# Optimization experiments

Measured on AMD Instinct MI355X. Metric: run time of the kernel, lower is better.

Reference implementation:

```python
import jax, jax.numpy as jnp
import numpy as np

B = 128      # graphs
N = 32       # atoms per graph (fixed)
NODES = B * N
E = B * N * N  # fully-connected edges incl. self-loops
H = 256      # hidden_dim
TD = 128     # time_dim
TYPE = 100   # type_dim
NF = 10      # frac_emb_freq
EDGE_DIM = NF * 2 * 3 + 6  # 66
L = 4        # num_layers
EPS = 1e-5


def _edges():
    idx = jnp.arange(NODES).reshape(B, N)
    ei = jnp.broadcast_to(idx[:, :, None], (B, N, N)).reshape(-1)  # row (target)
    ej = jnp.broadcast_to(idx[:, None, :], (B, N, N)).reshape(-1)  # col (source)
    return ei, ej


def _layernorm(x, g, b):
    mu = jnp.mean(x, axis=-1, keepdims=True)
    var = jnp.mean((x - mu) ** 2, axis=-1, keepdims=True)
    return (x - mu) * jax.lax.rsqrt(var + EPS) * g + b


def setup_inputs() -> dict:
    key = jax.random.key(0)
    ks = jax.random.split(key, 32)
    p = lambda k, shp: (jax.random.normal(k, shp, dtype=jnp.float32) * 0.02)
    inp = {
        "t": jax.random.uniform(ks[0], (B,), dtype=jnp.float32),
        "atom_types": jax.random.normal(ks[1], (NODES, TYPE), dtype=jnp.float32),
        "frac_coords": jax.random.uniform(ks[2], (NODES, 3), dtype=jnp.float32),
        "l_polar": jax.random.normal(ks[3], (B, 6), dtype=jnp.float32),
        "node2graph": jnp.repeat(jnp.arange(B, dtype=jnp.int32), N),
        # type_smooth
        "Ws": p(ks[4], (TYPE, H)), "bs": jnp.zeros((H,), jnp.float32),
        # node_embedding
        "Wn": p(ks[5], (H + TD, H)), "bn": jnp.zeros((H,), jnp.float32),
        # per-layer params, stacked over L
        "ln_g": jnp.ones((L, H), jnp.float32), "ln_b": jnp.zeros((L, H), jnp.float32),
        "m1_W": p(ks[6], (L, 2 * H + EDGE_DIM, H)), "m1_b": jnp.zeros((L, H), jnp.float32),
        "m2_W": p(ks[7], (L, H, H)), "m2_b": jnp.zeros((L, H), jnp.float32),
        "a1_W": p(ks[8], (L, 2 * H, H)), "a1_b": jnp.zeros((L, H), jnp.float32),
        "a2_W": p(ks[9], (L, H, H)), "a2_b": jnp.zeros((L, H), jnp.float32),
        # final layer norm + readouts
        "fln_g": jnp.ones((H,), jnp.float32), "fln_b": jnp.zeros((H,), jnp.float32),
        "type_W": p(ks[10], (H, TYPE)), "type_b": jnp.zeros((TYPE,), jnp.float32),
        "polar_W": p(ks[11], (H, 6)),
        "frac_W": p(ks[12], (H, 3)),
    }
    return inp


def reference(t, atom_types, frac_coords, l_polar, node2graph,
              Ws, bs, Wn, bn, ln_g, ln_b, m1_W, m1_b, m2_W, m2_b,
              a1_W, a1_b, a2_W, a2_b, fln_g, fln_b, type_W, type_b,
              polar_W, frac_W):
    ei, ej = _edges()
    edge2graph = node2graph[ei]

    # ---- node features: type_smooth + sinusoidal time embedding ----
    half = TD // 2
    tfreq = jnp.exp(jnp.arange(half, dtype=jnp.float32) * (-np.log(10000.0) / (half - 1)))
    targ = t[:, None] * tfreq[None, :]                       # [B, half]
    time_emb = jnp.concatenate([jnp.sin(targ), jnp.cos(targ)], axis=-1)  # [B, TD]
    time_emb = jnp.repeat(time_emb, N, axis=0)               # [NODES, TD]
    type_emb = atom_types @ Ws + bs                           # [NODES, H]
    nf = jnp.concatenate([type_emb, time_emb], axis=-1) @ Wn + bn  # [NODES, H]

    # ---- edge features: sinusoidal frac-diff embedding + l_polar ----
    d = jnp.mod(frac_coords[ej] - frac_coords[ei], 1.0)       # [E, 3]
    ffreq = 2.0 * np.pi * jnp.arange(NF, dtype=jnp.float32)
    femb = (d[:, :, None] * ffreq[None, None, :]).reshape(E, NF * 3)
    femb = jnp.concatenate([jnp.sin(femb), jnp.cos(femb)], axis=-1)  # [E, 60]
    ef = jnp.concatenate([femb, l_polar[edge2graph]], axis=-1)       # [E, 66]

    # ---- GNN layers ----
    ones = jnp.ones((E,), jnp.float32)
    cnt = jax.ops.segment_sum(ones, ei, num_segments=NODES)          # [NODES]
    cnt = jnp.maximum(cnt, 1.0)[:, None]
    for i in range(L):
        h = _layernorm(nf, ln_g[i], ln_b[i])
        mij = jnp.concatenate([h[ei], h[ej], ef], axis=-1)           # [E, 2H+66]
        mij = jax.nn.silu(mij @ m1_W[i] + m1_b[i])
        mij = jax.nn.silu(mij @ m2_W[i] + m2_b[i])                   # [E, H]
        msg = jax.ops.segment_sum(mij, ei, num_segments=NODES) / cnt  # scatter-mean
        a = jnp.concatenate([nf, msg], axis=-1)
        a = jax.nn.silu(a @ a1_W[i] + a1_b[i])
        a = jax.nn.silu(a @ a2_W[i] + a2_b[i])
        nf = nf + a

    nf = _layernorm(nf, fln_g, fln_b)
    gsum = jax.ops.segment_sum(nf, node2graph, num_segments=B)
    gcnt = jnp.maximum(jax.ops.segment_sum(jnp.ones((NODES,), jnp.float32), node2graph, num_segments=B), 1.0)
    graph_features = gsum / gcnt[:, None]

    type_pred = nf @ type_W + type_b
    l_polar_pred = graph_features @ polar_W
    frac_coords_pred = nf @ frac_W
    return type_pred, l_polar_pred, frac_coords_pred
```

## Files before the change

kernel.cpp:

```cpp
#include <hip/hip_runtime.h>
#include <hip/hip_bf16.h>

typedef __attribute__((ext_vector_type(8))) short short8;
typedef __attribute__((ext_vector_type(4))) short short4v;
typedef __attribute__((ext_vector_type(4))) float float4v;
typedef __bf16 bf16x8 __attribute__((ext_vector_type(8)));

#define MFMA16(A,B,C) __builtin_amdgcn_mfma_f32_16x16x32_bf16( \
    __builtin_bit_cast(bf16x8,(A)), __builtin_bit_cast(bf16x8,(B)), (C), 0, 0, 0)

static __device__ __forceinline__ float bf2f(unsigned short b){
  unsigned u = ((unsigned)b) << 16; float f; __builtin_memcpy(&f,&u,sizeof(f)); return f;
}
static __device__ __forceinline__ unsigned short f2bf(float f){
  unsigned u; __builtin_memcpy(&u,&f,sizeof(u));
  u = (u + 0x7FFFu + ((u>>16)&1u)) >> 16; return (unsigned short)u;
}
static __device__ __forceinline__ float siluf(float x){
  return x * __builtin_amdgcn_rcpf(1.0f + __expf(-x));
}
static __device__ __forceinline__ float ldf(const float* p, size_t i){ return p[i]; }
static __device__ __forceinline__ float ldf(const unsigned short* p, size_t i){ return bf2f(p[i]); }

__global__ __launch_bounds__(256) void k_gemm(
    const unsigned short* __restrict__ A, int lda,
    const unsigned short* __restrict__ Bp, int KT, int NT,
    const float* __restrict__ bias,
    float* __restrict__ outF, int ldoF,
    unsigned short* __restrict__ outH, int ldoH,
    const float* __restrict__ res,
    int Nc, int flags)
{
  const int w = threadIdx.x >> 6, lane = threadIdx.x & 63;
  const int l15 = lane & 15, q = lane >> 4;
  const int rowL = blockIdx.x * 64 + w * 16;
  const int colB = blockIdx.y * 64;
  const short8* pa = (const short8*)(A + (size_t)(rowL + l15) * lda);
  const short8* pb = (const short8*)Bp;
  float4v acc[4] = {};
  int ntc[4];
  #pragma unroll
  for (int i = 0; i < 4; ++i){ int t = (colB >> 4) + i; ntc[i] = t < NT ? t : NT - 1; }
  for (int kt = 0; kt < KT; ++kt){
    short8 a = pa[kt * 4 + q];
    #pragma unroll
    for (int i = 0; i < 4; ++i){
      short8 b = pb[(size_t)(kt * NT + ntc[i]) * 64 + lane];
      acc[i] = MFMA16(a, b, acc[i]);
    }
  }
  const bool doB = flags & 2, doS = flags & 1, doR = flags & 4;
  #pragma unroll
  for (int i = 0; i < 4; ++i){
    int c = colB + i * 16 + l15;
    if (c >= Nc) continue;
    float bv = doB ? bias[c] : 0.0f;
    #pragma unroll
    for (int r = 0; r < 4; ++r){
      int row = rowL + q * 4 + r;
      float v = acc[i][r] + bv;
      if (doS) v = siluf(v);
      if (doR) v += res[(size_t)row * ldoF + c];
      if (outF) outF[(size_t)row * ldoF + c] = v;
      if (outH) outH[(size_t)row * ldoH + c] = f2bf(v);
    }
  }
}

template<typename T>
static __device__ __forceinline__ void pack_tile(
    const T* W, int ldw, int Krows, int Ncols,
    unsigned short* dst, int NTtot, int ntoff, int kt, int nt,
    const float* addrow)
{
  int lane = threadIdx.x;
  int l15 = lane & 15, q = lane >> 4;
  int col = nt * 16 + l15;
  int kr0 = kt * 32 + q * 8;
  short8 v;
  #pragma unroll
  for (int j = 0; j < 8; ++j){
    int r = kr0 + j;
    float x = 0.0f;
    if (r < Krows && col < Ncols){
      x = ldf(W, (size_t)r * ldw + col);
      if (addrow) x += addrow[(r >> 5) * 256 + col];
    }
    v[j] = (short)f2bf(x);
  }
  ((short8*)dst)[(size_t)(kt * NTtot + ntoff + nt) * 64 + lane] = v;
}

__global__ void k_packW(
    const float* Ws, const float* Wn,
    const float* typeW, const float* polarW, const float* fracW,
    const float* m1W, const float* m2W, const float* a1W, const float* a2W,
    unsigned short* Wsp, unsigned short* Wnp, unsigned short* typep,
    unsigned short* polarp, unsigned short* fracp,
    unsigned short* W12p, unsigned short* W1botp, unsigned short* W2Tp,
    unsigned short* a1p, unsigned short* a2p)
{
  int b = blockIdx.x;
  if (b < 64)      { pack_tile(Ws,    256, 100, 256, Wsp,   16, 0, b >> 4, b & 15, nullptr); return; }
  if (b < 256){ int s = b - 64;  pack_tile(Wn,    256, 384, 256, Wnp,   16, 0, s >> 4, s & 15, nullptr); return; }
  if (b < 312){ int s = b - 256; pack_tile(typeW, 100, 256, 100, typep,  7, 0, s / 7,  s % 7,  nullptr); return; }
  if (b < 320){ int s = b - 312; pack_tile(polarW,  6, 256,   6, polarp, 1, 0, s, 0, nullptr); return; }
  if (b < 328){ int s = b - 320; pack_tile(fracW,   3, 256,   3, fracp,  1, 0, s, 0, nullptr); return; }
  int s2 = b - 328;
  int l = s2 / 800, bb = s2 % 800;
  const float* m1Wl = m1W + (size_t)l * 578 * 256;
  const float* m2Wl = m2W + (size_t)l * 65536;
  const float* a1Wl = a1W + (size_t)l * 131072;
  const float* a2Wl = a2W + (size_t)l * 65536;
  unsigned short* W12pl   = W12p   + (size_t)l * 131072;
  unsigned short* W1botpl = W1botp + (size_t)l * 16384;
  unsigned short* W2Tpl   = W2Tp   + (size_t)l * 65536;
  unsigned short* a1pl    = a1p    + (size_t)l * 131072;
  unsigned short* a2pl    = a2p    + (size_t)l * 65536;
  if (bb < 128)       pack_tile(m1Wl,           256, 256, 256, W12pl,  32,  0, bb >> 4, bb & 15, nullptr);
  else if (bb < 256){ int s = bb - 128; pack_tile(m1Wl + 256*256, 256, 256, 256, W12pl,  32, 16, s >> 4, s & 15, nullptr); }
  else if (bb < 288){ int s = bb - 256; pack_tile(m1Wl + 512*256, 256,  64, 256, W1botpl,16,  0, s >> 4, s & 15, nullptr); }
  else if (bb < 416){ int s = bb - 288; pack_tile(m2Wl,           256, 256, 256, W2Tpl,  16,  0, s >> 4, s & 15, nullptr); }
  else if (bb < 672){ int s = bb - 416; pack_tile(a1Wl,           256, 512, 256, a1pl,   16,  0, s >> 4, s & 15, nullptr); }
  else              { int s = bb - 672; pack_tile(a2Wl,           256, 256, 256, a2pl,   16,  0, s >> 4, s & 15, nullptr); }
}

__global__ void k_prep2(const float* at, const float* t, const float* fc,
                        const float* lpol, const float* m1W, const float* m1b,
                        unsigned short* atp, unsigned short* cat1,
                        unsigned short* femb, float* lpw)
{
  int b = blockIdx.x;
  if (b < 2048){
    int id = b * 256 + threadIdx.x;
    int r = id >> 7, c = id & 127;
    atp[id] = (c < 100) ? f2bf(at[r * 100 + c]) : (unsigned short)0;
  } else if (b < 2176){
    int g = b - 2048, i = threadIdx.x;
    if (i < 128){
      float tg = t[g];
      int f = i & 63;
      float fr = __expf((-9.210340371976184f / 63.0f) * (float)f);
      float arg = tg * fr;
      float v = (i < 64) ? __sinf(arg) : __cosf(arg);
      unsigned short hv = f2bf(v);
      for (int n = 0; n < 32; ++n)
        cat1[(size_t)(g * 32 + n) * 384 + 256 + i] = hv;
    }
  } else if (b < 2688){
    int e = (b - 2176) * 256 + threadIdx.x;
    int g = e >> 10, i = (e >> 5) & 31, j = e & 31;
    int nt = g * 32 + i, ns = g * 32 + j;
    unsigned short o[64];
    #pragma unroll
    for (int k = 0; k < 3; ++k){
      float d = fc[ns * 3 + k] - fc[nt * 3 + k];
      d -= floorf(d);
      #pragma unroll
      for (int f = 0; f < 10; ++f){
        float ang = d * (6.283185307179586f * (float)f);
        o[k * 10 + f]      = f2bf(__sinf(ang));
        o[30 + k * 10 + f] = f2bf(__cosf(ang));
      }
    }
    #pragma unroll
    for (int z = 60; z < 64; ++z) o[z] = 0;
    short8* dst = (short8*)(femb + (size_t)e * 64);
    #pragma unroll
    for (int v = 0; v < 8; ++v){
      short8 s;
      #pragma unroll
      for (int j2 = 0; j2 < 8; ++j2) s[j2] = (short)o[v * 8 + j2];
      dst[v] = s;
    }
  } else {
    int s = b - 2688;
    int l = s >> 7, g = s & 127, c = threadIdx.x;
    const float* W = m1W + (size_t)l * 578 * 256;
    float acc = m1b[l * 256 + c];
    #pragma unroll
    for (int k = 0; k < 6; ++k)
      acc += lpol[g * 6 + k] * W[(572 + k) * 256 + c];
    lpw[((size_t)l * 128 + g) * 256 + c] = acc;
  }
}

#define HLD 264

__global__ __launch_bounds__(256) void k_lnP(
    const float* __restrict__ nf, const float* __restrict__ g_,
    const float* __restrict__ b_,
    const unsigned short* __restrict__ W12p, const float* __restrict__ lpwl,
    unsigned short* __restrict__ P1Tp, unsigned short* __restrict__ P2Tp)
{
  __shared__ unsigned short hld[32 * HLD];
  __shared__ unsigned short PT[256 * 40];
  const int w = threadIdx.x >> 6, lane = threadIdx.x & 63;
  const int l15 = lane & 15, q = lane >> 4;
  const int g = blockIdx.x >> 1, halfT = blockIdx.x & 1;
  #pragma unroll
  for (int rr = 0; rr < 8; ++rr){
    int row = w * 8 + rr;
    float4v x = *(const float4v*)(nf + ((size_t)(g*32+row))*256 + lane*4);
    float s = x[0]+x[1]+x[2]+x[3];
    #pragma unroll
    for (int m=1;m<64;m<<=1) s += __shfl_xor(s,m,64);
    float mu = s * (1.f/256.f);
    float d0=x[0]-mu,d1=x[1]-mu,d2=x[2]-mu,d3=x[3]-mu;
    float vs=d0*d0+d1*d1+d2*d2+d3*d3;
    #pragma unroll
    for (int m=1;m<64;m<<=1) vs += __shfl_xor(vs,m,64);
    float rs = rsqrtf(vs*(1.f/256.f)+1e-5f);
    float4v gg = *(const float4v*)(g_ + lane*4);
    float4v bb = *(const float4v*)(b_ + lane*4);
    short4v o;
    o[0]=(short)f2bf(d0*rs*gg[0]+bb[0]);
    o[1]=(short)f2bf(d1*rs*gg[1]+bb[1]);
    o[2]=(short)f2bf(d2*rs*gg[2]+bb[2]);
    o[3]=(short)f2bf(d3*rs*gg[3]+bb[3]);
    *(short4v*)(&hld[row*HLD + lane*4]) = o;
  }
  __syncthreads();
  float4v acc[2][4] = {};
  const short8* pb = (const short8*)W12p;
  for (int kt = 0; kt < 8; ++kt){
    short8 a0 = *(const short8*)(&hld[(size_t)l15*HLD + kt*32 + q*8]);
    short8 a1 = *(const short8*)(&hld[(size_t)(16+l15)*HLD + kt*32 + q*8]);
    #pragma unroll
    for (int i = 0; i < 4; ++i){
      short8 bfr = pb[(size_t)(kt*32 + halfT*16 + w*4 + i)*64 + lane];
      acc[0][i] = MFMA16(a0, bfr, acc[0][i]);
      acc[1][i] = MFMA16(a1, bfr, acc[1][i]);
    }
  }
  #pragma unroll
  for (int i = 0; i < 4; ++i){
    int Tl = w*4 + i;
    float lv = (halfT == 0) ? lpwl[g*256 + Tl*16 + l15] : 0.0f;
    #pragma unroll
    for (int mt = 0; mt < 2; ++mt){
      short4v o;
      #pragma unroll
      for (int r = 0; r < 4; ++r) o[r] = (short)f2bf(acc[mt][i][r] + lv);
      *(short4v*)(&PT[(size_t)(Tl*16 + l15)*40 + mt*16 + q*4]) = o;
    }
  }
  __syncthreads();
  unsigned short* dstbase = halfT ? P2Tp : P1Tp;
  #pragma unroll
  for (int s = 0; s < 4; ++s){
    int Tl = w + s*4;
    short8 v = *(const short8*)(&PT[(size_t)(Tl*16 + l15)*40 + q*8]);
    *(short8*)(dstbase + ((size_t)(g*16 + Tl)*64 + lane)*8) = v;
  }
}

__global__ __launch_bounds__(256) void k_a12(
    const unsigned short* __restrict__ cat2,
    const unsigned short* __restrict__ a1pl, const float* __restrict__ a1bl,
    const unsigned short* __restrict__ a2pl, const float* __restrict__ a2bl,
    float* __restrict__ nf, unsigned short* __restrict__ cat2w)
{
  __shared__ unsigned short t1[16 * HLD];
  const int w = threadIdx.x >> 6, lane = threadIdx.x & 63;
  const int l15 = lane & 15, q = lane >> 4;
  const int r0 = blockIdx.x * 16;
  const short8* pb1 = (const short8*)a1pl;
  const short8* pb2 = (const short8*)a2pl;
  float4v acc[4] = {};
  for (int kt = 0; kt < 16; ++kt){
    short8 a0 = *(const short8*)(cat2 + (size_t)(r0 + l15)*512 + kt*32 + q*8);
    #pragma unroll
    for (int i = 0; i < 4; ++i){
      short8 bfr = pb1[(size_t)(kt*16 + w*4 + i)*64 + lane];
      acc[i] = MFMA16(a0, bfr, acc[i]);
    }
  }
  #pragma unroll
  for (int i = 0; i < 4; ++i){
    int c = (w*4+i)*16 + l15;
    float bv = a1bl[c];
    #pragma unroll
    for (int r = 0; r < 4; ++r)
      t1[(size_t)(q*4 + r)*HLD + c] = f2bf(siluf(acc[i][r] + bv));
  }
  __syncthreads();
  float4v c2[4] = {};
  for (int kt = 0; kt < 8; ++kt){
    short8 a0 = *(const short8*)(&t1[(size_t)l15*HLD + kt*32 + q*8]);
    #pragma unroll
    for (int i = 0; i < 4; ++i){
      short8 bfr = pb2[(size_t)(kt*16 + w*4 + i)*64 + lane];
      c2[i] = MFMA16(a0, bfr, c2[i]);
    }
  }
  #pragma unroll
  for (int i = 0; i < 4; ++i){
    int c = (w*4+i)*16 + l15;
    float bv = a2bl[c];
    #pragma unroll
    for (int r = 0; r < 4; ++r){
      int row = r0 + q*4 + r;
      float v = nf[(size_t)row*256 + c] + siluf(c2[i][r] + bv);
      nf[(size_t)row*256 + c] = v;
      cat2w[(size_t)row*512 + c] = f2bf(v);
    }
  }
}

__global__ __launch_bounds__(256) void k_lnF(
    const float* __restrict__ nf, const float* __restrict__ g_,
    const float* __restrict__ b_,
    unsigned short* __restrict__ h, unsigned short* __restrict__ gf)
{
  __shared__ unsigned short hld[32 * HLD];
  const int w = threadIdx.x >> 6, lane = threadIdx.x & 63;
  const int g = blockIdx.x;
  #pragma unroll
  for (int rr = 0; rr < 8; ++rr){
    int row = w * 8 + rr;
    float4v x = *(const float4v*)(nf + ((size_t)(g*32+row))*256 + lane*4);
    float s = x[0]+x[1]+x[2]+x[3];
    #pragma unroll
    for (int m=1;m<64;m<<=1) s += __shfl_xor(s,m,64);
    float mu = s * (1.f/256.f);
    float d0=x[0]-mu,d1=x[1]-mu,d2=x[2]-mu,d3=x[3]-mu;
    float vs=d0*d0+d1*d1+d2*d2+d3*d3;
    #pragma unroll
    for (int m=1;m<64;m<<=1) vs += __shfl_xor(vs,m,64);
    float rs = rsqrtf(vs*(1.f/256.f)+1e-5f);
    float4v gg = *(const float4v*)(g_ + lane*4);
    float4v bb = *(const float4v*)(b_ + lane*4);
    short4v o;
    o[0]=(short)f2bf(d0*rs*gg[0]+bb[0]);
    o[1]=(short)f2bf(d1*rs*gg[1]+bb[1]);
    o[2]=(short)f2bf(d2*rs*gg[2]+bb[2]);
    o[3]=(short)f2bf(d3*rs*gg[3]+bb[3]);
    *(short4v*)(&hld[row*HLD + lane*4]) = o;
    *(short4v*)(h + ((size_t)(g*32+row))*256 + lane*4) = o;
  }
  __syncthreads();
  int c = threadIdx.x;
  float s = 0.0f;
  #pragma unroll
  for (int n = 0; n < 32; ++n) s += bf2f(hld[n*HLD + c]);
  gf[g*256 + c] = f2bf(s * (1.0f/32.0f));
}

#define EST 268
__global__ __launch_bounds__(256, 4) void k_edge(
    const unsigned short* __restrict__ femb,
    const unsigned short* __restrict__ W1botp,
    const unsigned short* __restrict__ P1Tp,
    const unsigned short* __restrict__ P2Tp,
    const unsigned short* __restrict__ W2Tp,
    const float* __restrict__ b2,
    unsigned short* __restrict__ cat2)
{
  __shared__ unsigned short M1[64 * EST];
  const int w = threadIdx.x >> 6, lane = threadIdx.x & 63;
  const int l15 = lane & 15, q = lane >> 4;
  const int b = blockIdx.x, g = b >> 4;
  const int n0 = (b & 15) * 2;
  const int cb = w * 64;
  const short8* fb8  = (const short8*)femb;
  const short8* w1b8 = (const short8*)W1botp;
  const short8* p1t8 = (const short8*)P1Tp;
  const short8* p2t8 = (const short8*)P2Tp;
  const short8* w2t8 = (const short8*)W2Tp;

  short8 ohj[2], ohn[2];
  #pragma unroll
  for (int p = 0; p < 2; ++p){
    int tj = p * 16 + l15;
    int tn = n0 + p;
    #pragma unroll
    for (int j = 0; j < 8; ++j){
      ohj[p][j] = (short)((q * 8 + j) == tj ? 0x3F80 : 0);
      ohn[p][j] = (short)((q * 8 + j) == tn ? 0x3F80 : 0);
    }
  }

  float4v acc[4][4] = {};
  #pragma unroll
  for (int ks = 0; ks < 4; ++ks){
    short8 a[4];
    #pragma unroll
    for (int ct = 0; ct < 4; ++ct){
      int nt = w * 4 + ct;
      if (ks < 2)       a[ct] = w1b8[(size_t)(ks * 16 + nt) * 64 + lane];
      else if (ks == 2) a[ct] = p2t8[(size_t)(g * 16 + nt) * 64 + lane];
      else              a[ct] = p1t8[(size_t)(g * 16 + nt) * 64 + lane];
    }
    #pragma unroll
    for (int et = 0; et < 4; ++et){
      short8 bf;
      if (ks < 2){
        int edge = b * 64 + et * 16 + l15;
        bf = fb8[(size_t)edge * 8 + ks * 4 + q];
      } else if (ks == 2) bf = ohj[et & 1];
      else                bf = ohn[et >> 1];
      #pragma unroll
      for (int ct = 0; ct < 4; ++ct)
        acc[ct][et] = MFMA16(a[ct], bf, acc[ct][et]);
    }
  }
  #pragma unroll
  for (int ct = 0; ct < 4; ++ct)
    #pragma unroll
    for (int et = 0; et < 4; ++et){
      short4v sv;
      #pragma unroll
      for (int r = 0; r < 4; ++r) sv[r] = (short)f2bf(siluf(acc[ct][et][r]));
      *(short4v*)(&M1[(size_t)(et * 16 + l15) * EST + cb + ct * 16 + q * 4]) = sv;
    }
  __syncthreads();
  float4v c2[4][4] = {};
  for (int kt = 0; kt < 8; ++kt){
    short8 a[4];
    #pragma unroll
    for (int ct = 0; ct < 4; ++ct)
      a[ct] = w2t8[(size_t)(kt * 16 + w * 4 + ct) * 64 + lane];
    #pragma unroll
    for (int et = 0; et < 4; ++et){
      short8 bf = *(const short8*)(&M1[(size_t)(et * 16 + l15) * EST + kt * 32 + q * 8]);
      #pragma unroll
      for (int ct = 0; ct < 4; ++ct)
        c2[ct][et] = MFMA16(a[ct], bf, c2[ct][et]);
    }
  }
  float bv[4][4];
  #pragma unroll
  for (int ct = 0; ct < 4; ++ct)
    #pragma unroll
    for (int r = 0; r < 4; ++r) bv[ct][r] = b2[cb + ct * 16 + q * 4 + r];
  #pragma unroll
  for (int nn = 0; nn < 2; ++nn){
    #pragma unroll
    for (int ct = 0; ct < 4; ++ct){
      #pragma unroll
      for (int r = 0; r < 4; ++r){
        float v = siluf(c2[ct][2*nn][r] + bv[ct][r])
                + siluf(c2[ct][2*nn+1][r] + bv[ct][r]);
        v += __shfl_xor(v, 1, 16);
        v += __shfl_xor(v, 2, 16);
        v += __shfl_xor(v, 4, 16);
        v += __shfl_xor(v, 8, 16);
        if (l15 == 0)
          cat2[(size_t)(b*2 + nn) * 512 + 256 + cb + ct * 16 + q * 4 + r] =
              f2bf(v * (1.0f / 32.0f));
      }
    }
  }
}

extern "C" void kernel_launch(void* const* d_in, const int* in_sizes, int n_in,
                              void* d_out, int out_size, void* d_ws, size_t ws_size,
                              hipStream_t stream)
{
  const float* t      = (const float*)d_in[0];
  const float* at     = (const float*)d_in[1];
  const float* fc     = (const float*)d_in[2];
  const float* lpol   = (const float*)d_in[3];
  const float* Ws     = (const float*)d_in[5];
  const float* bs     = (const float*)d_in[6];
  const float* Wn     = (const float*)d_in[7];
  const float* bn     = (const float*)d_in[8];
  const float* ln_g   = (const float*)d_in[9];
  const float* ln_b   = (const float*)d_in[10];
  const float* m1W    = (const float*)d_in[11];
  const float* m1b    = (const float*)d_in[12];
  const float* m2W    = (const float*)d_in[13];
  const float* m2b    = (const float*)d_in[14];
  const float* a1W    = (const float*)d_in[15];
  const float* a1b    = (const float*)d_in[16];
  const float* a2W    = (const float*)d_in[17];
  const float* a2b    = (const float*)d_in[18];
  const float* flng   = (const float*)d_in[19];
  const float* flnb   = (const float*)d_in[20];
  const float* typeW  = (const float*)d_in[21];
  const float* typeb  = (const float*)d_in[22];
  const float* polarW = (const float*)d_in[23];
  const float* fracW  = (const float*)d_in[24];
  float* out = (float*)d_out;

  char* ws = (char*)d_ws;
  size_t off = 0;
  auto alloc = [&](size_t bytes) -> char* {
    char* p = ws + off; off += (bytes + 255) & ~(size_t)255; return p;
  };
  float*          nf    = (float*)         alloc((size_t)4096*256*4);
  unsigned short* cat2  = (unsigned short*)alloc((size_t)4096*512*2);
  unsigned short* h     = (unsigned short*)alloc((size_t)4096*256*2);
  unsigned short* cat1  = (unsigned short*)alloc((size_t)4096*384*2);
  unsigned short* atp   = (unsigned short*)alloc((size_t)4096*128*2);
  unsigned short* femb  = (unsigned short*)alloc((size_t)131072*64*2);
  float*          lpw   = (float*)         alloc((size_t)4*128*256*4);
  unsigned short* P1Tp  = (unsigned short*)alloc((size_t)128*16*64*8*2);
  unsigned short* P2Tp  = (unsigned short*)alloc((size_t)128*16*64*8*2);
  unsigned short* gf    = (unsigned short*)alloc((size_t)128*256*2);
  unsigned short* Wsp   = (unsigned short*)alloc((size_t)4*16*1024);
  unsigned short* Wnp   = (unsigned short*)alloc((size_t)12*16*1024);
  unsigned short* typep = (unsigned short*)alloc((size_t)8*7*1024);
  unsigned short* polarp= (unsigned short*)alloc((size_t)8*1*1024);
  unsigned short* fracp = (unsigned short*)alloc((size_t)8*1*1024);
  unsigned short* W12p  = (unsigned short*)alloc((size_t)4*131072*2);
  unsigned short* W1botp= (unsigned short*)alloc((size_t)4*16384*2);
  unsigned short* W2Tp  = (unsigned short*)alloc((size_t)4*65536*2);
  unsigned short* a1p   = (unsigned short*)alloc((size_t)4*131072*2);
  unsigned short* a2p   = (unsigned short*)alloc((size_t)4*65536*2);

  k_packW<<<dim3(3528), dim3(64), 0, stream>>>(Ws, Wn, typeW, polarW, fracW,
      m1W, m2W, a1W, a2W,
      Wsp, Wnp, typep, polarp, fracp, W12p, W1botp, W2Tp, a1p, a2p);
  k_prep2<<<dim3(3200), dim3(256), 0, stream>>>(at, t, fc, lpol, m1W, m1b,
                                                atp, cat1, femb, lpw);
  k_gemm<<<dim3(64,4), dim3(256), 0, stream>>>(atp, 128, Wsp, 4, 16, bs,
      (float*)nullptr, 0, cat1, 384, (const float*)nullptr, 256, 2);
  k_gemm<<<dim3(64,4), dim3(256), 0, stream>>>(cat1, 384, Wnp, 12, 16, bn,
      nf, 256, cat2, 512, (const float*)nullptr, 256, 2);

  for (int l = 0; l < 4; ++l){
    k_lnP<<<dim3(256), dim3(256), 0, stream>>>(nf, ln_g + l*256, ln_b + l*256,
        W12p + (size_t)l*131072, lpw + (size_t)l*32768, P1Tp, P2Tp);
    k_edge<<<dim3(2048), dim3(256), 0, stream>>>(femb, W1botp + (size_t)l*16384,
        P1Tp, P2Tp, W2Tp + (size_t)l*65536, m2b + l*256, cat2);
    k_a12<<<dim3(256), dim3(256), 0, stream>>>(cat2, a1p + (size_t)l*131072,
        a1b + l*256, a2p + (size_t)l*65536, a2b + l*256, nf, cat2);
  }

  k_lnF<<<dim3(128), dim3(256), 0, stream>>>(nf, flng, flnb, h, gf);
  k_gemm<<<dim3(64,2), dim3(256), 0, stream>>>(h, 256, typep, 8, 7, typeb,
      out, 100, (unsigned short*)nullptr, 0, (const float*)nullptr, 100, 2);
  k_gemm<<<dim3(2,1), dim3(256), 0, stream>>>(gf, 256, polarp, 8, 1,
      (const float*)nullptr, out + 409600, 6, (unsigned short*)nullptr, 0,
      (const float*)nullptr, 6, 0);
  k_gemm<<<dim3(64,1), dim3(256), 0, stream>>>(h, 256, fracp, 8, 1,
      (const float*)nullptr, out + 410368, 3, (unsigned short*)nullptr, 0,
      (const float*)nullptr, 3, 0);
}
```

Before: 396.6 us.

## Fuse node MLP update with next layer's layernorm and projection kernel

```diff
diff --git a/kernel.cpp b/kernel.cpp
--- a/kernel.cpp
+++ b/kernel.cpp
@@ -255,25 +255,34 @@
   }
 }
 
-__global__ __launch_bounds__(256) void k_a12(
+__global__ __launch_bounds__(256, 2) void k_alnP(
     const unsigned short* __restrict__ cat2,
     const unsigned short* __restrict__ a1pl, const float* __restrict__ a1bl,
     const unsigned short* __restrict__ a2pl, const float* __restrict__ a2bl,
-    float* __restrict__ nf, unsigned short* __restrict__ cat2w)
-{
-  __shared__ unsigned short t1[16 * HLD];
+    float* __restrict__ nf, unsigned short* __restrict__ cat2w,
+    const float* __restrict__ g_, const float* __restrict__ b_,
+    const unsigned short* __restrict__ W12p, const float* __restrict__ lpwl,
+    unsigned short* __restrict__ P1Tp, unsigned short* __restrict__ P2Tp)
+{
+  __shared__ unsigned short t1[32 * HLD];
+  __shared__ float red[32][4], redq[32][4];
+  __shared__ float mu32[32], rs32[32];
+  __shared__ unsigned short hld[32 * HLD];
+  __shared__ unsigned short PT[256 * 40];
   const int w = threadIdx.x >> 6, lane = threadIdx.x & 63;
   const int l15 = lane & 15, q = lane >> 4;
-  const int r0 = blockIdx.x * 16;
+  const int g = blockIdx.x, r0 = g * 32;
   const short8* pb1 = (const short8*)a1pl;
   const short8* pb2 = (const short8*)a2pl;
-  float4v acc[4] = {};
+  float4v acc[2][4] = {};
   for (int kt = 0; kt < 16; ++kt){
     short8 a0 = *(const short8*)(cat2 + (size_t)(r0 + l15)*512 + kt*32 + q*8);
+    short8 a1 = *(const short8*)(cat2 + (size_t)(r0 + 16 + l15)*512 + kt*32 + q*8);
     #pragma unroll
     for (int i = 0; i < 4; ++i){
       short8 bfr = pb1[(size_t)(kt*16 + w*4 + i)*64 + lane];
-      acc[i] = MFMA16(a0, bfr, acc[i]);
+      acc[0][i] = MFMA16(a0, bfr, acc[0][i]);
+      acc[1][i] = MFMA16(a1, bfr, acc[1][i]);
     }
   }
   #pragma unroll
@@ -281,63 +290,223 @@
     int c = (w*4+i)*16 + l15;
     float bv = a1bl[c];
     #pragma unroll
-    for (int r = 0; r < 4; ++r)
-      t1[(size_t)(q*4 + r)*HLD + c] = f2bf(siluf(acc[i][r] + bv));
-  }
-  __syncthreads();
-  float4v c2[4] = {};
+    for (int mt = 0; mt < 2; ++mt)
+      #pragma unroll
+      for (int r = 0; r < 4; ++r)
+        t1[(size_t)(mt*16 + q*4 + r)*HLD + c] = f2bf(siluf(acc[mt][i][r] + bv));
+  }
+  __syncthreads();
+  float4v c2[2][4] = {};
   for (int kt = 0; kt < 8; ++kt){
     short8 a0 = *(const short8*)(&t1[(size_t)l15*HLD + kt*32 + q*8]);
+    short8 a1 = *(const short8*)(&t1[(size_t)(16 + l15)*HLD + kt*32 + q*8]);
     #pragma unroll
     for (int i = 0; i < 4; ++i){
       short8 bfr = pb2[(size_t)(kt*16 + w*4 + i)*64 + lane];
-      c2[i] = MFMA16(a0, bfr, c2[i]);
-    }
-  }
+      c2[0][i] = MFMA16(a0, bfr, c2[0][i]);
+      c2[1][i] = MFMA16(a1, bfr, c2[1][i]);
+    }
+  }
+  float v[2][4][4];
   #pragma unroll
   for (int i = 0; i < 4; ++i){
     int c = (w*4+i)*16 + l15;
     float bv = a2bl[c];
     #pragma unroll
+    for (int mt = 0; mt < 2; ++mt)
+      #pragma unroll
+      for (int r = 0; r < 4; ++r){
+        int row = r0 + mt*16 + q*4 + r;
+        float vv = nf[(size_t)row*256 + c] + siluf(c2[mt][i][r] + bv);
+        v[mt][i][r] = vv;
+        nf[(size_t)row*256 + c] = vv;
+        cat2w[(size_t)row*512 + c] = f2bf(vv);
+      }
+  }
+  #pragma unroll
+  for (int mt = 0; mt < 2; ++mt)
+    #pragma unroll
     for (int r = 0; r < 4; ++r){
-      int row = r0 + q*4 + r;
-      float v = nf[(size_t)row*256 + c] + siluf(c2[i][r] + bv);
-      nf[(size_t)row*256 + c] = v;
-      cat2w[(size_t)row*512 + c] = f2bf(v);
-    }
-  }
-}
-
-__global__ __launch_bounds__(256) void k_lnF(
-    const float* __restrict__ nf, const float* __restrict__ g_,
-    const float* __restrict__ b_,
+      float s  = v[mt][0][r] + v[mt][1][r] + v[mt][2][r] + v[mt][3][r];
+      float sq = v[mt][0][r]*v[mt][0][r] + v[mt][1][r]*v[mt][1][r]
+               + v[mt][2][r]*v[mt][2][r] + v[mt][3][r]*v[mt][3][r];
+      #pragma unroll
+      for (int m = 1; m < 16; m <<= 1){
+        s  += __shfl_xor(s,  m, 16);
+        sq += __shfl_xor(sq, m, 16);
+      }
+      if (l15 == 0){
+        int row = mt*16 + q*4 + r;
+        red[row][w]  = s;
+        redq[row][w] = sq;
+      }
+    }
+  __syncthreads();
+  if (threadIdx.x < 32){
+    int row = threadIdx.x;
+    float s  = red[row][0]  + red[row][1]  + red[row][2]  + red[row][3];
+    float sq = redq[row][0] + redq[row][1] + redq[row][2] + redq[row][3];
+    float mu = s * (1.0f/256.0f);
+    float var = sq * (1.0f/256.0f) - mu*mu;
+    mu32[row] = mu;
+    rs32[row] = rsqrtf(var + 1e-5f);
+  }
+  __syncthreads();
+  #pragma unroll
+  for (int i = 0; i < 4; ++i){
+    int c = (w*4+i)*16 + l15;
+    float gv = g_[c], bv = b_[c];
+    #pragma unroll
+    for (int mt = 0; mt < 2; ++mt)
+      #pragma unroll
+      for (int r = 0; r < 4; ++r){
+        int row = mt*16 + q*4 + r;
+        hld[(size_t)row*HLD + c] = f2bf((v[mt][i][r] - mu32[row]) * rs32[row] * gv + bv);
+      }
+  }
+  __syncthreads();
+  const short8* pb = (const short8*)W12p;
+  for (int halfT = 0; halfT < 2; ++halfT){
+    float4v pacc[2][4] = {};
+    for (int kt = 0; kt < 8; ++kt){
+      short8 a0 = *(const short8*)(&hld[(size_t)l15*HLD + kt*32 + q*8]);
+      short8 a1 = *(const short8*)(&hld[(size_t)(16+l15)*HLD + kt*32 + q*8]);
+      #pragma unroll
+      for (int i = 0; i < 4; ++i){
+        short8 bfr = pb[(size_t)(kt*32 + halfT*16 + w*4 + i)*64 + lane];
+        pacc[0][i] = MFMA16(a0, bfr, pacc[0][i]);
+        pacc[1][i] = MFMA16(a1, bfr, pacc[1][i]);
+      }
+    }
+    #pragma unroll
+    for (int i = 0; i < 4; ++i){
+      int Tl = w*4 + i;
+      float lv = (halfT == 0) ? lpwl[g*256 + Tl*16 + l15] : 0.0f;
+      #pragma unroll
+      for (int mt = 0; mt < 2; ++mt){
+        short4v o;
+        #pragma unroll
+        for (int r = 0; r < 4; ++r) o[r] = (short)f2bf(pacc[mt][i][r] + lv);
+        *(short4v*)(&PT[(size_t)(Tl*16 + l15)*40 + mt*16 + q*4]) = o;
+      }
+    }
+    __syncthreads();
+    unsigned short* dstbase = halfT ? P2Tp : P1Tp;
+    #pragma unroll
+    for (int s = 0; s < 4; ++s){
+      int Tl = w + s*4;
+      short8 vv = *(const short8*)(&PT[(size_t)(Tl*16 + l15)*40 + q*8]);
+      *(short8*)(dstbase + ((size_t)(g*16 + Tl)*64 + lane)*8) = vv;
+    }
+    __syncthreads();
+  }
+}
+
+__global__ __launch_bounds__(256, 2) void k_alnF(
+    const unsigned short* __restrict__ cat2,
+    const unsigned short* __restrict__ a1pl, const float* __restrict__ a1bl,
+    const unsigned short* __restrict__ a2pl, const float* __restrict__ a2bl,
+    const float* __restrict__ nf,
+    const float* __restrict__ g_, const float* __restrict__ b_,
     unsigned short* __restrict__ h, unsigned short* __restrict__ gf)
 {
+  __shared__ unsigned short t1[32 * HLD];
+  __shared__ float red[32][4], redq[32][4];
+  __shared__ float mu32[32], rs32[32];
   __shared__ unsigned short hld[32 * HLD];
   const int w = threadIdx.x >> 6, lane = threadIdx.x & 63;
-  const int g = blockIdx.x;
-  #pragma unroll
-  for (int rr = 0; rr < 8; ++rr){
-    int row = w * 8 + rr;
-    float4v x = *(const float4v*)(nf + ((size_t)(g*32+row))*256 + lane*4);
-    float s = x[0]+x[1]+x[2]+x[3];
-    #pragma unroll
-    for (int m=1;m<64;m<<=1) s += __shfl_xor(s,m,64);
-    float mu = s * (1.f/256.f);
-    float d0=x[0]-mu,d1=x[1]-mu,d2=x[2]-mu,d3=x[3]-mu;
-    float vs=d0*d0+d1*d1+d2*d2+d3*d3;
-    #pragma unroll
-    for (int m=1;m<64;m<<=1) vs += __shfl_xor(vs,m,64);
-    float rs = rsqrtf(vs*(1.f/256.f)+1e-5f);
-    float4v gg = *(const float4v*)(g_ + lane*4);
-    float4v bb = *(const float4v*)(b_ + lane*4);
-    short4v o;
-    o[0]=(short)f2bf(d0*rs*gg[0]+bb[0]);
-    o[1]=(short)f2bf(d1*rs*gg[1]+bb[1]);
-    o[2]=(short)f2bf(d2*rs*gg[2]+bb[2]);
-    o[3]=(short)f2bf(d3*rs*gg[3]+bb[3]);
-    *(short4v*)(&hld[row*HLD + lane*4]) = o;
-    *(short4v*)(h + ((size_t)(g*32+row))*256 + lane*4) = o;
+  const int l15 = lane & 15, q = lane >> 4;
+  const int g = blockIdx.x, r0 = g * 32;
+  const short8* pb1 = (const short8*)a1pl;
+  const short8* pb2 = (const short8*)a2pl;
+  float4v acc[2][4] = {};
+  for (int kt = 0; kt < 16; ++kt){
+    short8 a0 = *(const short8*)(cat2 + (size_t)(r0 + l15)*512 + kt*32 + q*8);
+    short8 a1 = *(const short8*)(cat2 + (size_t)(r0 + 16 + l15)*512 + kt*32 + q*8);
+    #pragma unroll
+    for (int i = 0; i < 4; ++i){
+      short8 bfr = pb1[(size_t)(kt*16 + w*4 + i)*64 + lane];
+      acc[0][i] = MFMA16(a0, bfr, acc[0][i]);
+      acc[1][i] = MFMA16(a1, bfr, acc[1][i]);
+    }
+  }
+  #pragma unroll
+  for (int i = 0; i < 4; ++i){
+    int c = (w*4+i)*16 + l15;
+    float bv = a1bl[c];
+    #pragma unroll
+    for (int mt = 0; mt < 2; ++mt)
+      #pragma unroll
+      for (int r = 0; r < 4; ++r)
+        t1[(size_t)(mt*16 + q*4 + r)*HLD + c] = f2bf(siluf(acc[mt][i][r] + bv));
+  }
+  __syncthreads();
+  float4v c2[2][4] = {};
+  for (int kt = 0; kt < 8; ++kt){
+    short8 a0 = *(const short8*)(&t1[(size_t)l15*HLD + kt*32 + q*8]);
+    short8 a1 = *(const short8*)(&t1[(size_t)(16 + l15)*HLD + kt*32 + q*8]);
+    #pragma unroll
+    for (int i = 0; i < 4; ++i){
+      short8 bfr = pb2[(size_t)(kt*16 + w*4 + i)*64 + lane];
+      c2[0][i] = MFMA16(a0, bfr, c2[0][i]);
+      c2[1][i] = MFMA16(a1, bfr, c2[1][i]);
+    }
+  }
+  float v[2][4][4];
+  #pragma unroll
+  for (int i = 0; i < 4; ++i){
+    int c = (w*4+i)*16 + l15;
+    float bv = a2bl[c];
+    #pragma unroll
+    for (int mt = 0; mt < 2; ++mt)
+      #pragma unroll
+      for (int r = 0; r < 4; ++r){
+        int row = r0 + mt*16 + q*4 + r;
+        v[mt][i][r] = nf[(size_t)row*256 + c] + siluf(c2[mt][i][r] + bv);
+      }
+  }
+  #pragma unroll
+  for (int mt = 0; mt < 2; ++mt)
+    #pragma unroll
+    for (int r = 0; r < 4; ++r){
+      float s  = v[mt][0][r] + v[mt][1][r] + v[mt][2][r] + v[mt][3][r];
+      float sq = v[mt][0][r]*v[mt][0][r] + v[mt][1][r]*v[mt][1][r]
+               + v[mt][2][r]*v[mt][2][r] + v[mt][3][r]*v[mt][3][r];
+      #pragma unroll
+      for (int m = 1; m < 16; m <<= 1){
+        s  += __shfl_xor(s,  m, 16);
+        sq += __shfl_xor(sq, m, 16);
+      }
+      if (l15 == 0){
+        int row = mt*16 + q*4 + r;
+        red[row][w]  = s;
+        redq[row][w] = sq;
+      }
+    }
+  __syncthreads();
+  if (threadIdx.x < 32){
+    int row = threadIdx.x;
+    float s  = red[row][0]  + red[row][1]  + red[row][2]  + red[row][3];
+    float sq = redq[row][0] + redq[row][1] + redq[row][2] + redq[row][3];
+    float mu = s * (1.0f/256.0f);
+    float var = sq * (1.0f/256.0f) - mu*mu;
+    mu32[row] = mu;
+    rs32[row] = rsqrtf(var + 1e-5f);
+  }
+  __syncthreads();
+  #pragma unroll
+  for (int i = 0; i < 4; ++i){
+    int c = (w*4+i)*16 + l15;
+    float gv = g_[c], bv = b_[c];
+    #pragma unroll
+    for (int mt = 0; mt < 2; ++mt)
+      #pragma unroll
+      for (int r = 0; r < 4; ++r){
+        int row = mt*16 + q*4 + r;
+        unsigned short hv = f2bf((v[mt][i][r] - mu32[row]) * rs32[row] * gv + bv);
+        hld[(size_t)row*HLD + c] = hv;
+        h[(size_t)(r0 + row)*256 + c] = hv;
+      }
   }
   __syncthreads();
   int c = threadIdx.x;
@@ -348,7 +517,7 @@
 }
 
 #define EST 268
-__global__ __launch_bounds__(256, 4) void k_edge(
+__global__ __launch_bounds__(256, 2) void k_edge(
     const unsigned short* __restrict__ femb,
     const unsigned short* __restrict__ W1botp,
     const unsigned short* __restrict__ P1Tp,
@@ -520,16 +689,22 @@
   k_gemm<<<dim3(64,4), dim3(256), 0, stream>>>(cat1, 384, Wnp, 12, 16, bn,
       nf, 256, cat2, 512, (const float*)nullptr, 256, 2);
 
+  k_lnP<<<dim3(256), dim3(256), 0, stream>>>(nf, ln_g, ln_b, W12p, lpw, P1Tp, P2Tp);
   for (int l = 0; l < 4; ++l){
-    k_lnP<<<dim3(256), dim3(256), 0, stream>>>(nf, ln_g + l*256, ln_b + l*256,
-        W12p + (size_t)l*131072, lpw + (size_t)l*32768, P1Tp, P2Tp);
     k_edge<<<dim3(2048), dim3(256), 0, stream>>>(femb, W1botp + (size_t)l*16384,
         P1Tp, P2Tp, W2Tp + (size_t)l*65536, m2b + l*256, cat2);
-    k_a12<<<dim3(256), dim3(256), 0, stream>>>(cat2, a1p + (size_t)l*131072,
-        a1b + l*256, a2p + (size_t)l*65536, a2b + l*256, nf, cat2);
-  }
-
-  k_lnF<<<dim3(128), dim3(256), 0, stream>>>(nf, flng, flnb, h, gf);
+    if (l < 3){
+      k_alnP<<<dim3(128), dim3(256), 0, stream>>>(cat2,
+          a1p + (size_t)l*131072, a1b + l*256, a2p + (size_t)l*65536, a2b + l*256,
+          nf, cat2, ln_g + (l+1)*256, ln_b + (l+1)*256,
+          W12p + (size_t)(l+1)*131072, lpw + (size_t)(l+1)*32768, P1Tp, P2Tp);
+    } else {
+      k_alnF<<<dim3(128), dim3(256), 0, stream>>>(cat2,
+          a1p + (size_t)l*131072, a1b + l*256, a2p + (size_t)l*65536, a2b + l*256,
+          nf, flng, flnb, h, gf);
+    }
+  }
+
   k_gemm<<<dim3(64,2), dim3(256), 0, stream>>>(h, 256, typep, 8, 7, typeb,
       out, 100, (unsigned short*)nullptr, 0, (const float*)nullptr, 100, 2);
   k_gemm<<<dim3(2,1), dim3(256), 0, stream>>>(gf, 256, polarp, 8, 1,
```

After: 460.9 us. 16.2% more time.
